# Kernel tuning notes

Measured on AMD Instinct MI355X. Metric: run time of the kernel, lower is better.

Reference implementation:

```python
import jax, jax.numpy as jnp
import numpy as np

N = 100_000   # active voxels
CIN = 64
COUT = 64
K = 3
L = 128       # voxel grid extent per axis
C = K // 2    # kernel center


def _offsets():
    # spatial offsets (z, y, x) for all non-center kernel taps, in the same
    # enumeration order as the original module's triple loop
    offs = []
    for dz in range(K):
        for dy in range(K):
            for dx in range(K):
                if (dz, dy, dx) != (C, C, C):
                    offs.append((dz - C, dy - C, dx - C))
    return offs


def _build_neighbor_map(coords):
    # coords: [N,3] int, unique. For each offset build (out_idx, in_idx) pairs
    # where voxel out_idx has an active neighbor in_idx at coords+offset.
    keys = (coords[:, 0].astype(np.int64) * L + coords[:, 1]) * L + coords[:, 2]
    order = np.argsort(keys)
    skeys = keys[order]
    pairs = []
    for (z, y, x) in _offsets():
        nb = coords + np.array([z, y, x], dtype=coords.dtype)
        valid = np.all((nb >= 0) & (nb < L), axis=1)
        nkeys = (nb[:, 0].astype(np.int64) * L + nb[:, 1]) * L + nb[:, 2]
        pos = np.clip(np.searchsorted(skeys, nkeys), 0, N - 1)
        found = valid & (skeys[pos] == nkeys)
        out_idx = np.nonzero(found)[0].astype(np.int32)
        in_idx = order[pos[found]].astype(np.int32)
        pairs.append((out_idx, in_idx))
    P = max(len(o) for o, _ in pairs)
    nei = np.zeros((len(pairs), P, 2), dtype=np.int32)
    sizes = np.zeros(len(pairs), dtype=np.int32)
    for i, (o, j) in enumerate(pairs):
        nei[i, :len(o), 0] = o
        nei[i, :len(o), 1] = j
        sizes[i] = len(o)
    return nei, sizes


def setup_inputs() -> dict:
    rng = np.random.default_rng(0)
    flat = rng.choice(L * L * L, size=N, replace=False)  # unique voxel coords
    coords = np.stack([flat // (L * L), (flat // L) % L, flat % L], axis=1).astype(np.int32)
    nei, sizes = _build_neighbor_map(coords)
    key = jax.random.key(0)
    k1, k2, k3 = jax.random.split(key, 3)
    sp_values = jax.random.normal(k1, (N, CIN), dtype=jnp.float32)
    weight = jax.random.normal(k2, (COUT, K, K, K, CIN), dtype=jnp.float32) * 0.05
    bias = jax.random.normal(k3, (COUT,), dtype=jnp.float32)
    return {"sp_values": sp_values, "weight": weight, "bias": bias,
            "nei_indices": jnp.asarray(nei), "nei_sizes": jnp.asarray(sizes)}


def reference(sp_values, weight, bias, nei_indices, nei_sizes):
    # weight: [Cout,kz,ky,kx,Cin] -> [kz,ky,kx,Cin,Cout] (matches torch permute)
    w = jnp.transpose(weight, (1, 2, 3, 4, 0))
    out = sp_values @ w[C, C, C]                                   # center tap: [N,Cout]
    offs = _offsets()
    w_offs = jnp.stack([w[z + C, y + C, x + C] for (z, y, x) in offs])  # [O,Cin,Cout]
    P = nei_indices.shape[1]
    valid = (jnp.arange(P)[None, :] < nei_sizes[:, None]).astype(sp_values.dtype)  # [O,P]
    gathered = sp_values[nei_indices[:, :, 1]] * valid[:, :, None]  # [O,P,Cin], padded rows zeroed
    contrib = jnp.einsum('opc,ocd->opd', gathered, w_offs)          # [O,P,Cout]
    out = out.at[nei_indices[:, :, 0].reshape(-1)].add(contrib.reshape(-1, out.shape[1]))
    return out + bias
```

## Files before the change

### kernel.cpp

```cpp
#include <hip/hip_runtime.h>


typedef __bf16 bf16x8 __attribute__((ext_vector_type(8)));
typedef float f32x4 __attribute__((ext_vector_type(4)));

#define LDSP 72

__device__ __forceinline__ unsigned short f2bf(float f) {
    union { float f; unsigned int u; } v; v.f = f;
    unsigned int u = v.u;
    return (unsigned short)((u + 0x7FFFu + ((u >> 16) & 1u)) >> 16);
}

__device__ __forceinline__ ushort4 cvt4(float4 v) {
    ushort4 b;
    b.x = f2bf(v.x); b.y = f2bf(v.y); b.z = f2bf(v.z); b.w = f2bf(v.w);
    return b;
}

__global__ __launch_bounds__(256) void sp3d_center(
    const float* __restrict__ sp, const float* __restrict__ w,
    const float* __restrict__ bias, float* __restrict__ out, int n_rows)
{
    __shared__ unsigned short Alds[64 * LDSP];
    __shared__ unsigned short Wlds[64 * LDSP];
    const int t = threadIdx.x;
    const int row0 = blockIdx.x * 64;

    for (int i = 0; i < 4; ++i) {
        int f4 = t + 256 * i;
        int n = f4 >> 4, k = (f4 & 15) << 2;
        float4 v = *(const float4*)&w[n * 1728 + 832 + k];
        *(ushort4*)&Wlds[n * LDSP + k] = cvt4(v);
    }
    {
        int r = t >> 2, q = t & 3;
        long rowg = row0 + r;
        if (rowg >= n_rows) rowg = n_rows - 1;
        for (int i = 0; i < 4; ++i) {
            int col = q * 4 + i * 16;
            float4 v = *(const float4*)&sp[rowg * 64 + col];
            *(ushort4*)&Alds[r * LDSP + col] = cvt4(v);
        }
    }
    __syncthreads();

    const int wid = t >> 6, lane = t & 63, ml = lane & 15, quad = lane >> 4;
    const bf16x8 a0 = *(const bf16x8*)&Alds[(wid * 16 + ml) * LDSP + quad * 8];
    const bf16x8 a1 = *(const bf16x8*)&Alds[(wid * 16 + ml) * LDSP + 32 + quad * 8];
    f32x4 acc[4];
    #pragma unroll
    for (int nt = 0; nt < 4; ++nt) {
        bf16x8 b0 = *(const bf16x8*)&Wlds[(nt * 16 + ml) * LDSP + quad * 8];
        bf16x8 b1 = *(const bf16x8*)&Wlds[(nt * 16 + ml) * LDSP + 32 + quad * 8];
        acc[nt] = f32x4{0.f, 0.f, 0.f, 0.f};
        acc[nt] = __builtin_amdgcn_mfma_f32_16x16x32_bf16(a0, b0, acc[nt], 0, 0, 0);
        acc[nt] = __builtin_amdgcn_mfma_f32_16x16x32_bf16(a1, b1, acc[nt], 0, 0, 0);
    }
    #pragma unroll
    for (int nt = 0; nt < 4; ++nt) {
        int col = nt * 16 + ml;
        float bv = bias[col];
        #pragma unroll
        for (int rg = 0; rg < 4; ++rg) {
            int row = row0 + wid * 16 + quad * 4 + rg;
            if (row < n_rows) out[row * 64 + col] = acc[nt][rg] + bv;
        }
    }
}

__global__ __launch_bounds__(256) void sp3d_scatter(
    const float* __restrict__ sp, const float* __restrict__ w,
    const int* __restrict__ nei, const int* __restrict__ sizes,
    float* __restrict__ out, int P)
{
    __shared__ unsigned short Alds[64 * LDSP];
    __shared__ unsigned short Wlds[64 * LDSP];
    __shared__ int sO[64];
    __shared__ int sI[64];

    const int o = blockIdx.y;
    const int size_o = sizes[o];
    const int chunk = blockIdx.x * 64;
    if (chunk >= size_o) return;
    const int t = threadIdx.x;
    const int tap = o + (o >= 13 ? 1 : 0);

    if (t < 64) {
        int p = chunk + t;
        if (p < size_o) {
            int2 pr = *(const int2*)&nei[(o * P + p) * 2];
            sO[t] = pr.x; sI[t] = pr.y;
        } else { sO[t] = -1; sI[t] = 0; }
    }
    for (int i = 0; i < 4; ++i) {
        int f4 = t + 256 * i;
        int n = f4 >> 4, k = (f4 & 15) << 2;
        float4 v = *(const float4*)&w[n * 1728 + tap * 64 + k];
        *(ushort4*)&Wlds[n * LDSP + k] = cvt4(v);
    }
    __syncthreads();

    {
        int r = t >> 2, q = t & 3;
        long rowg = sI[r];
        for (int i = 0; i < 4; ++i) {
            int col = q * 4 + i * 16;
            float4 v = *(const float4*)&sp[rowg * 64 + col];
            *(ushort4*)&Alds[r * LDSP + col] = cvt4(v);
        }
    }
    __syncthreads();

    const int wid = t >> 6, lane = t & 63, ml = lane & 15, quad = lane >> 4;
    const bf16x8 a0 = *(const bf16x8*)&Alds[(wid * 16 + ml) * LDSP + quad * 8];
    const bf16x8 a1 = *(const bf16x8*)&Alds[(wid * 16 + ml) * LDSP + 32 + quad * 8];
    f32x4 acc[4];
    #pragma unroll
    for (int nt = 0; nt < 4; ++nt) {
        bf16x8 b0 = *(const bf16x8*)&Wlds[(nt * 16 + ml) * LDSP + quad * 8];
        bf16x8 b1 = *(const bf16x8*)&Wlds[(nt * 16 + ml) * LDSP + 32 + quad * 8];
        acc[nt] = f32x4{0.f, 0.f, 0.f, 0.f};
        acc[nt] = __builtin_amdgcn_mfma_f32_16x16x32_bf16(a0, b0, acc[nt], 0, 0, 0);
        acc[nt] = __builtin_amdgcn_mfma_f32_16x16x32_bf16(a1, b1, acc[nt], 0, 0, 0);
    }
    #pragma unroll
    for (int nt = 0; nt < 4; ++nt) {
        int col = nt * 16 + ml;
        #pragma unroll
        for (int rg = 0; rg < 4; ++rg) {
            int rowl = wid * 16 + quad * 4 + rg;
            int go = sO[rowl];
            if (go >= 0) atomicAdd(&out[go * 64 + col], acc[nt][rg]);
        }
    }
}

extern "C" void kernel_launch(void* const* d_in, const int* in_sizes, int n_in,
                              void* d_out, int out_size, void* d_ws, size_t ws_size,
                              hipStream_t stream) {
    const float* sp    = (const float*)d_in[0];
    const float* w     = (const float*)d_in[1];
    const float* bias  = (const float*)d_in[2];
    const int*   nei   = (const int*)d_in[3];
    const int*   sizes = (const int*)d_in[4];
    float* out = (float*)d_out;

    const int N = in_sizes[0] / 64;
    const int P = in_sizes[3] / (26 * 2);

    dim3 g1((N + 63) / 64);
    sp3d_center<<<g1, 256, 0, stream>>>(sp, w, bias, out, N);

    dim3 g2((P + 63) / 64, 26);
    sp3d_scatter<<<g2, 256, 0, stream>>>(sp, w, nei, sizes, out, P);
}
```

Baseline: 116.3 us.

## Fuse center and scatter taps into output-tiled kernel with LDS accumulation

Replaces the separate center GEMM and per-offset global-atomic scatter kernels with a prep kernel and a single main kernel. The prep kernel converts all weights to bf16 once and binary-searches per-offset segment starts for each 128-row output tile. It relies on out_idx being sorted within each offset list. The main kernel computes the center tap into an LDS accumulator, then each wave walks the neighbor pairs for its offsets, gathers inputs, runs MFMA and accumulates with LDS atomics, and writes the tile once with bias. This removes global atomics and repeated weight conversion. In exchange, parallelism is reduced to one block per output tile, and gather rows are processed one 16-row group at a time per wave.

```diff
diff --git a/kernel.cpp b/kernel.cpp
--- a/kernel.cpp
+++ b/kernel.cpp
@@ -4,7 +4,9 @@
 typedef __bf16 bf16x8 __attribute__((ext_vector_type(8)));
 typedef float f32x4 __attribute__((ext_vector_type(4)));
 
-#define LDSP 72
+#define TROWS 128
+#define LDSA 72
+#define OSTR 68
 
 __device__ __forceinline__ unsigned short f2bf(float f) {
     union { float f; unsigned int u; } v; v.f = f;
@@ -18,120 +20,161 @@
     return b;
 }
 
-__global__ __launch_bounds__(256) void sp3d_center(
-    const float* __restrict__ sp, const float* __restrict__ w,
-    const float* __restrict__ bias, float* __restrict__ out, int n_rows)
+__global__ __launch_bounds__(256) void sp3d_prep(
+    const float* __restrict__ w, const int* __restrict__ nei,
+    const int* __restrict__ sizes, unsigned short* __restrict__ wbf,
+    int* __restrict__ starts, int P, int T, int wblocks)
 {
-    __shared__ unsigned short Alds[64 * LDSP];
-    __shared__ unsigned short Wlds[64 * LDSP];
+    const int b = blockIdx.x;
+    if (b < wblocks) {
+        int id = b * 256 + threadIdx.x;
+        if (id < 27 * 64 * 16) {
+            int k4 = id & 15, n = (id >> 4) & 63, tap = id >> 10;
+            float4 v = *(const float4*)&w[n * 1728 + tap * 64 + k4 * 4];
+            *(ushort4*)&wbf[(tap * 64 + n) * 64 + k4 * 4] = cvt4(v);
+        }
+    } else {
+        int id = (b - wblocks) * 256 + threadIdx.x;
+        if (id < 26 * (T + 1)) {
+            int t = id % (T + 1), o = id / (T + 1);
+            int target = t * TROWS;
+            int lo = 0, hi = sizes[o];
+            while (lo < hi) {
+                int mid = (lo + hi) >> 1;
+                if (nei[(o * P + mid) * 2] < target) lo = mid + 1; else hi = mid;
+            }
+            starts[o * (T + 1) + t] = lo;
+        }
+    }
+}
+
+__global__ __launch_bounds__(256, 2) void sp3d_main(
+    const float* __restrict__ sp, const float* __restrict__ bias,
+    const int* __restrict__ nei, const unsigned short* __restrict__ wbf,
+    const int* __restrict__ starts, float* __restrict__ out,
+    int N, int P, int T)
+{
+    __shared__ unsigned short A[TROWS * LDSA];
+    __shared__ float Ol[TROWS * OSTR];
+    __shared__ unsigned short Ap[4][16 * LDSA];
+
     const int t = threadIdx.x;
-    const int row0 = blockIdx.x * 64;
-
-    for (int i = 0; i < 4; ++i) {
-        int f4 = t + 256 * i;
-        int n = f4 >> 4, k = (f4 & 15) << 2;
-        float4 v = *(const float4*)&w[n * 1728 + 832 + k];
-        *(ushort4*)&Wlds[n * LDSP + k] = cvt4(v);
-    }
-    {
-        int r = t >> 2, q = t & 3;
-        long rowg = row0 + r;
-        if (rowg >= n_rows) rowg = n_rows - 1;
-        for (int i = 0; i < 4; ++i) {
-            int col = q * 4 + i * 16;
-            float4 v = *(const float4*)&sp[rowg * 64 + col];
-            *(ushort4*)&Alds[r * LDSP + col] = cvt4(v);
+    const int w = t >> 6, lane = t & 63, ml = lane & 15, quad = lane >> 4;
+    const int row0 = blockIdx.x * TROWS;
+    const __bf16* Wg = (const __bf16*)wbf;
+
+    {
+        int r = t >> 2, c4 = t & 3;
+        for (int g = 0; g < 2; ++g) {
+            int rl = r + g * 64;
+            long rowg = row0 + rl; if (rowg >= N) rowg = N - 1;
+            #pragma unroll
+            for (int i = 0; i < 4; ++i) {
+                int col = (c4 + i * 4) * 4;
+                float4 v = *(const float4*)&sp[rowg * 64 + col];
+                *(ushort4*)&A[rl * LDSA + col] = cvt4(v);
+            }
         }
     }
     __syncthreads();
 
-    const int wid = t >> 6, lane = t & 63, ml = lane & 15, quad = lane >> 4;
-    const bf16x8 a0 = *(const bf16x8*)&Alds[(wid * 16 + ml) * LDSP + quad * 8];
-    const bf16x8 a1 = *(const bf16x8*)&Alds[(wid * 16 + ml) * LDSP + 32 + quad * 8];
-    f32x4 acc[4];
-    #pragma unroll
-    for (int nt = 0; nt < 4; ++nt) {
-        bf16x8 b0 = *(const bf16x8*)&Wlds[(nt * 16 + ml) * LDSP + quad * 8];
-        bf16x8 b1 = *(const bf16x8*)&Wlds[(nt * 16 + ml) * LDSP + 32 + quad * 8];
-        acc[nt] = f32x4{0.f, 0.f, 0.f, 0.f};
-        acc[nt] = __builtin_amdgcn_mfma_f32_16x16x32_bf16(a0, b0, acc[nt], 0, 0, 0);
-        acc[nt] = __builtin_amdgcn_mfma_f32_16x16x32_bf16(a1, b1, acc[nt], 0, 0, 0);
-    }
-    #pragma unroll
-    for (int nt = 0; nt < 4; ++nt) {
-        int col = nt * 16 + ml;
-        float bv = bias[col];
+    {
+        bf16x8 bf[4][2];
         #pragma unroll
-        for (int rg = 0; rg < 4; ++rg) {
-            int row = row0 + wid * 16 + quad * 4 + rg;
-            if (row < n_rows) out[row * 64 + col] = acc[nt][rg] + bv;
-        }
-    }
-}
-
-__global__ __launch_bounds__(256) void sp3d_scatter(
-    const float* __restrict__ sp, const float* __restrict__ w,
-    const int* __restrict__ nei, const int* __restrict__ sizes,
-    float* __restrict__ out, int P)
-{
-    __shared__ unsigned short Alds[64 * LDSP];
-    __shared__ unsigned short Wlds[64 * LDSP];
-    __shared__ int sO[64];
-    __shared__ int sI[64];
-
-    const int o = blockIdx.y;
-    const int size_o = sizes[o];
-    const int chunk = blockIdx.x * 64;
-    if (chunk >= size_o) return;
-    const int t = threadIdx.x;
-    const int tap = o + (o >= 13 ? 1 : 0);
-
-    if (t < 64) {
-        int p = chunk + t;
-        if (p < size_o) {
-            int2 pr = *(const int2*)&nei[(o * P + p) * 2];
-            sO[t] = pr.x; sI[t] = pr.y;
-        } else { sO[t] = -1; sI[t] = 0; }
-    }
-    for (int i = 0; i < 4; ++i) {
-        int f4 = t + 256 * i;
-        int n = f4 >> 4, k = (f4 & 15) << 2;
-        float4 v = *(const float4*)&w[n * 1728 + tap * 64 + k];
-        *(ushort4*)&Wlds[n * LDSP + k] = cvt4(v);
+        for (int nt = 0; nt < 4; ++nt)
+            #pragma unroll
+            for (int kh = 0; kh < 2; ++kh)
+                bf[nt][kh] = *(const bf16x8*)&Wg[(13 * 64 + nt * 16 + ml) * 64 + kh * 32 + quad * 8];
+        #pragma unroll
+        for (int mt = 0; mt < 2; ++mt) {
+            const __bf16* Ab = (const __bf16*)A + (w * 32 + mt * 16 + ml) * LDSA + quad * 8;
+            bf16x8 a0 = *(const bf16x8*)Ab;
+            bf16x8 a1 = *(const bf16x8*)(Ab + 32);
+            #pragma unroll
+            for (int nt = 0; nt < 4; ++nt) {
+                f32x4 acc = {0.f, 0.f, 0.f, 0.f};
+                acc = __builtin_amdgcn_mfma_f32_16x16x32_bf16(a0, bf[nt][0], acc, 0, 0, 0);
+                acc = __builtin_amdgcn_mfma_f32_16x16x32_bf16(a1, bf[nt][1], acc, 0, 0, 0);
+                #pragma unroll
+                for (int rg = 0; rg < 4; ++rg)
+                    Ol[(w * 32 + mt * 16 + quad * 4 + rg) * OSTR + nt * 16 + ml] = acc[rg];
+            }
+        }
     }
     __syncthreads();
 
     {
-        int r = t >> 2, q = t & 3;
-        long rowg = sI[r];
-        for (int i = 0; i < 4; ++i) {
-            int col = q * 4 + i * 16;
-            float4 v = *(const float4*)&sp[rowg * 64 + col];
-            *(ushort4*)&Alds[r * LDSP + col] = cvt4(v);
+        __bf16* ApW = (__bf16*)Ap[w];
+        for (int o = w; o < 26; o += 4) {
+            int lo = starts[o * (T + 1) + blockIdx.x];
+            int hi = starts[o * (T + 1) + blockIdx.x + 1];
+            if (lo >= hi) continue;
+            int tap = o + (o >= 13 ? 1 : 0);
+            bf16x8 bf[4][2];
+            #pragma unroll
+            for (int nt = 0; nt < 4; ++nt)
+                #pragma unroll
+                for (int kh = 0; kh < 2; ++kh)
+                    bf[nt][kh] = *(const bf16x8*)&Wg[(tap * 64 + nt * 16 + ml) * 64 + kh * 32 + quad * 8];
+
+            for (int base = lo; base < hi; base += 16) {
+                int cnt = hi - base; if (cnt > 16) cnt = 16;
+                int pr = lane >> 2, part = lane & 3;
+                int outl_v = -1;
+                if (pr < cnt) {
+                    int2 e = *(const int2*)&nei[((long)o * P + base + pr) * 2];
+                    outl_v = e.x - row0;
+                    long inrow = e.y;
+                    #pragma unroll
+                    for (int i = 0; i < 4; ++i) {
+                        float4 v = *(const float4*)&sp[inrow * 64 + part * 16 + i * 4];
+                        *(ushort4*)&ApW[pr * LDSA + part * 16 + i * 4] = cvt4(v);
+                    }
+                } else {
+                    ushort4 z = {0, 0, 0, 0};
+                    #pragma unroll
+                    for (int i = 0; i < 4; ++i)
+                        *(ushort4*)&ApW[pr * LDSA + part * 16 + i * 4] = z;
+                }
+                __asm__ __volatile__("s_waitcnt lgkmcnt(0)" ::: "memory");
+                bf16x8 a0 = *(const bf16x8*)&ApW[ml * LDSA + quad * 8];
+                bf16x8 a1 = *(const bf16x8*)&ApW[ml * LDSA + 32 + quad * 8];
+                #pragma unroll
+                for (int nt = 0; nt < 4; ++nt) {
+                    f32x4 acc = {0.f, 0.f, 0.f, 0.f};
+                    acc = __builtin_amdgcn_mfma_f32_16x16x32_bf16(a0, bf[nt][0], acc, 0, 0, 0);
+                    acc = __builtin_amdgcn_mfma_f32_16x16x32_bf16(a1, bf[nt][1], acc, 0, 0, 0);
+                    #pragma unroll
+                    for (int rg = 0; rg < 4; ++rg) {
+                        int slot = quad * 4 + rg;
+                        int ol = __shfl(outl_v, slot * 4);
+                        if (ol >= 0)
+                            atomicAdd(&Ol[ol * OSTR + nt * 16 + ml], acc[rg]);
+                    }
+                }
+            }
         }
     }
     __syncthreads();
 
-    const int wid = t >> 6, lane = t & 63, ml = lane & 15, quad = lane >> 4;
-    const bf16x8 a0 = *(const bf16x8*)&Alds[(wid * 16 + ml) * LDSP + quad * 8];
-    const bf16x8 a1 = *(const bf16x8*)&Alds[(wid * 16 + ml) * LDSP + 32 + quad * 8];
-    f32x4 acc[4];
-    #pragma unroll
-    for (int nt = 0; nt < 4; ++nt) {
-        bf16x8 b0 = *(const bf16x8*)&Wlds[(nt * 16 + ml) * LDSP + quad * 8];
-        bf16x8 b1 = *(const bf16x8*)&Wlds[(nt * 16 + ml) * LDSP + 32 + quad * 8];
-        acc[nt] = f32x4{0.f, 0.f, 0.f, 0.f};
-        acc[nt] = __builtin_amdgcn_mfma_f32_16x16x32_bf16(a0, b0, acc[nt], 0, 0, 0);
-        acc[nt] = __builtin_amdgcn_mfma_f32_16x16x32_bf16(a1, b1, acc[nt], 0, 0, 0);
-    }
-    #pragma unroll
-    for (int nt = 0; nt < 4; ++nt) {
-        int col = nt * 16 + ml;
-        #pragma unroll
-        for (int rg = 0; rg < 4; ++rg) {
-            int rowl = wid * 16 + quad * 4 + rg;
-            int go = sO[rowl];
-            if (go >= 0) atomicAdd(&out[go * 64 + col], acc[nt][rg]);
+    {
+        int r = t >> 2, c4 = t & 3;
+        for (int g = 0; g < 2; ++g) {
+            int rl = r + g * 64;
+            long rowg = row0 + rl;
+            if (rowg < N) {
+                #pragma unroll
+                for (int i = 0; i < 4; ++i) {
+                    int col = (c4 + i * 4) * 4;
+                    float4 bv = *(const float4*)&bias[col];
+                    float4 res;
+                    res.x = Ol[rl * OSTR + col + 0] + bv.x;
+                    res.y = Ol[rl * OSTR + col + 1] + bv.y;
+                    res.z = Ol[rl * OSTR + col + 2] + bv.z;
+                    res.w = Ol[rl * OSTR + col + 3] + bv.w;
+                    *(float4*)&out[rowg * 64 + col] = res;
+                }
+            }
         }
     }
 }
@@ -147,11 +190,14 @@
     float* out = (float*)d_out;
 
     const int N = in_sizes[0] / 64;
-    const int P = in_sizes[3] / (26 * 2);
-
-    dim3 g1((N + 63) / 64);
-    sp3d_center<<<g1, 256, 0, stream>>>(sp, w, bias, out, N);
-
-    dim3 g2((P + 63) / 64, 26);
-    sp3d_scatter<<<g2, 256, 0, stream>>>(sp, w, nei, sizes, out, P);
-}
+    const int P = in_sizes[3] / 52;
+    const int T = (N + TROWS - 1) / TROWS;
+
+    unsigned short* wbf = (unsigned short*)d_ws;
+    int* starts = (int*)((char*)d_ws + 27 * 64 * 64 * 2);
+
+    const int wblocks = (27 * 64 * 16 + 255) / 256;
+    const int sblocks = (26 * (T + 1) + 255) / 256;
+    sp3d_prep<<<wblocks + sblocks, 256, 0, stream>>>(w, nei, sizes, wbf, starts, P, T, wblocks);
+    sp3d_main<<<T, 256, 0, stream>>>(sp, bias, nei, wbf, starts, out, N, P, T);
+}
```

Result: slower. 154.7 us (+33.1%).
